# Performance work log

Hardware: AMD Instinct MI355X
Metric: run time of the kernel (lower is better)

The kernel has to match this reference:

```python
import jax, jax.numpy as jnp
import numpy as np

OBS_LEN = 20   # decoder timesteps
NC = 2         # n_coordinates
D = 64         # z_dim + s_dim (LSTM hidden size)
K = 20         # number of latent samples (len(pred_lstm_hidden))
N = 50000      # number of agents
H_MID = 32     # mapping MLP hidden dim


def setup_inputs() -> dict:
    key = jax.random.key(0)
    ks = jax.random.split(key, 8)
    return {
        "obs_traj_rel": jax.random.normal(ks[0], (OBS_LEN, N, NC), jnp.float32),
        "pred_lstm_hidden": jax.random.normal(ks[1], (K, N, D), jnp.float32),
        # mapping MLP: Linear(D->32) + LeakyReLU, Linear(32->D)
        "map_w1": jax.random.normal(ks[2], (H_MID, D), jnp.float32) * 0.1,
        "map_b1": jnp.zeros((H_MID,), jnp.float32),
        "map_w2": jax.random.normal(ks[3], (D, H_MID), jnp.float32) * 0.1,
        "map_b2": jnp.zeros((D,), jnp.float32),
        # LSTMCell params (weights ~ N(0, 0.1), biases zero per _initialize_weights)
        "w_ih": jax.random.normal(ks[4], (4 * D, NC), jnp.float32) * 0.1,
        "w_hh": jax.random.normal(ks[5], (4 * D, D), jnp.float32) * 0.1,
        "b_ih": jnp.zeros((4 * D,), jnp.float32),
        "b_hh": jnp.zeros((4 * D,), jnp.float32),
        # pred_hidden2pos: Linear(D -> NC)
        "pos_w": jax.random.normal(ks[6], (NC, D), jnp.float32) * 0.1,
        "pos_b": jnp.zeros((NC,), jnp.float32),
    }


def _hardsigmoid(x):
    # F.hardsigmoid: relu6(x + 3) / 6
    return jnp.clip(x / 6.0 + 0.5, 0.0, 1.0)


def _hardtanh(x):
    return jnp.clip(x, -1.0, 1.0)


def reference(obs_traj_rel, pred_lstm_hidden, map_w1, map_b1, map_w2, map_b2,
              w_ih, w_hh, b_ih, b_hh, pos_w, pos_b):
    # mapping MLP on initial hidden state: [K, N, D]
    h0 = jax.nn.leaky_relu(pred_lstm_hidden @ map_w1.T + map_b1, negative_slope=0.01)
    h0 = h0 @ map_w2.T + map_b2
    c0 = jnp.zeros_like(h0)

    # input at step i uses obs_traj_rel[max(i-1, 0)]
    idx = jnp.concatenate([jnp.zeros((1,), jnp.int32),
                           jnp.arange(OBS_LEN - 1, dtype=jnp.int32)])
    xs = obs_traj_rel[idx, :, :NC]  # [T, N, NC]

    def step(carry, x_t):
        h, c = carry                                   # [K, N, D]
        xb = jnp.broadcast_to(x_t, (K,) + x_t.shape)   # repeat over samples
        gates = xb @ w_ih.T + b_ih + h @ w_hh.T + b_hh  # [K, N, 4D]
        i_g, f_g, g_g, o_g = jnp.split(gates, 4, axis=-1)
        c_new = _hardsigmoid(f_g) * c + _hardsigmoid(i_g) * _hardtanh(g_g)
        h_new = _hardsigmoid(o_g) * _hardtanh(c_new)
        out = h_new @ pos_w.T + pos_b                  # [K, N, NC]
        return (h_new, c_new), out

    _, outs = jax.lax.scan(step, (h0, c0), xs)
    return outs  # [T, K, N, NC]
```

## Files before the change

kernel.cpp:

```cpp
#include <hip/hip_runtime.h>

#define T_STEPS 20
#define KK      20
#define NW      50000
#define DD      64

typedef __attribute__((ext_vector_type(8))) short bfx8;
typedef __attribute__((ext_vector_type(4))) short sx4;
typedef __attribute__((ext_vector_type(4))) float fx4;
typedef __attribute__((ext_vector_type(2))) float fx2;
typedef __attribute__((ext_vector_type(2))) int   ix2;
typedef __attribute__((ext_vector_type(4))) int   ix4;

__device__ __forceinline__ short f2bf(float f){
  unsigned u = __builtin_bit_cast(unsigned, f);
  return (short)((u + 0x7FFFu + ((u >> 16) & 1u)) >> 16);
}
__device__ __forceinline__ unsigned cvtpk(float lo, float hi){
  unsigned r; asm("v_cvt_pk_bf16_f32 %0, %1, %2" : "=v"(r) : "v"(lo), "v"(hi)); return r;
}
__device__ __forceinline__ float hsig(float x){
  return __builtin_amdgcn_fmed3f(fmaf(x, 0.16666667f, 0.5f), 0.f, 1.f);
}
__device__ __forceinline__ float htanh(float x){
  return __builtin_amdgcn_fmed3f(x, -1.f, 1.f);
}

__device__ __forceinline__ bfx8 frag_f32(const float* p0, const float* p1){
  fx4 lo = *(const fx4*)p0, hi = *(const fx4*)p1;
  bfx8 r;
  r[0]=f2bf(lo[0]); r[1]=f2bf(lo[1]); r[2]=f2bf(lo[2]); r[3]=f2bf(lo[3]);
  r[4]=f2bf(hi[0]); r[5]=f2bf(hi[1]); r[6]=f2bf(hi[2]); r[7]=f2bf(hi[3]);
  return r;
}
__device__ __forceinline__ bfx8 frag_lds(const unsigned short* p0, const unsigned short* p1){
  sx4 lo = *(const sx4*)p0, hi = *(const sx4*)p1;
  bfx8 r;
  r[0]=lo[0]; r[1]=lo[1]; r[2]=lo[2]; r[3]=lo[3];
  r[4]=hi[0]; r[5]=hi[1]; r[6]=hi[2]; r[7]=hi[3];
  return r;
}
__device__ __forceinline__ bfx8 cat(ix2 lo, ix2 hi){
  ix4 t; t[0]=lo[0]; t[1]=lo[1]; t[2]=hi[0]; t[3]=hi[1];
  return __builtin_bit_cast(bfx8, t);
}

#define MFMA(A,B,C) __builtin_amdgcn_mfma_f32_16x16x32_bf16((A),(B),(C),0,0,0)

__global__ __launch_bounds__(256)
void gcrl_fused(const float* __restrict__ obs, const float* __restrict__ pred,
                const float* __restrict__ w1, const float* __restrict__ b1,
                const float* __restrict__ w2, const float* __restrict__ b2,
                const float* __restrict__ wih, const float* __restrict__ whh,
                const float* __restrict__ bih, const float* __restrict__ bhh,
                const float* __restrict__ posw, const float* __restrict__ posb,
                float* __restrict__ out)
{
  __shared__ unsigned short hst[2][2][1152];
  __shared__ unsigned short l1buf[2][16][36];
  __shared__ float xs[19][8][2];

  const int tid = threadIdx.x;
  const int w   = tid >> 6;
  const int l   = tid & 63;
  const int g   = l >> 4;
  const int cc  = l & 15;

  const int bid = blockIdx.x;
  const int k0  = (bid % 5) * 4;
  const int n0  = (bid / 5) * 8;

  for (int i = tid; i < 19 * 16; i += 256){
    int row = i >> 4, rr = i & 15;
    xs[row][rr >> 1][rr & 1] =
      obs[(size_t)row * (NW * 2) + (size_t)(n0 + (rr >> 1)) * 2 + (rr & 1)];
  }

  bfx8 wf[4][2];
  bfx8 a2f[4];
  fx4  bs[4];
  #pragma unroll
  for (int ty = 0; ty < 4; ++ty){
    const int jrow = ty * 64 + w * 16 + cc;
    #pragma unroll
    for (int kt = 0; kt < 2; ++kt)
      wf[ty][kt] = frag_f32(&whh[jrow * DD + kt * 32 + g * 4],
                            &whh[jrow * DD + kt * 32 + 16 + g * 4]);
    unsigned xw = cvtpk(wih[jrow * 2 + 0], wih[jrow * 2 + 1]);
    ix4 t4; t4[0] = (g == 0) ? (int)xw : 0; t4[1] = 0; t4[2] = 0; t4[3] = 0;
    a2f[ty] = __builtin_bit_cast(bfx8, t4);
    const int jreg = ty * 64 + w * 16 + g * 4;
    bs[ty][0] = bih[jreg + 0] + bhh[jreg + 0];
    bs[ty][1] = bih[jreg + 1] + bhh[jreg + 1];
    bs[ty][2] = bih[jreg + 2] + bhh[jreg + 2];
    bs[ty][3] = bih[jreg + 3] + bhh[jreg + 3];
  }
  const int c2 = (cc < 2) ? cc : 0;
  bfx8 pf[2];
  #pragma unroll
  for (int kt = 0; kt < 2; ++kt)
    pf[kt] = frag_f32(&posw[c2 * DD + kt * 32 + g * 4],
                      &posw[c2 * DD + kt * 32 + 16 + g * 4]);
  fx4 pC; pC[0] = posb[0]; pC[1] = posb[1]; pC[2] = 0.f; pC[3] = 0.f;

  float* const outBase =
    out + ((size_t)(k0 + (cc & 3)) * NW + n0 + w * 4 + (cc >> 2)) * 2;

  if (w < 2){
    const int tl = w;
    const int kcell = k0 + (cc & 3);
    const int ncell = n0 + tl * 4 + (cc >> 2);
    const float* Pr = pred + ((size_t)kcell * NW + ncell) * DD;
    bfx8 pa0 = frag_f32(&Pr[g * 4],      &Pr[16 + g * 4]);
    bfx8 pa1 = frag_f32(&Pr[32 + g * 4], &Pr[48 + g * 4]);
    #pragma unroll
    for (int nt = 0; nt < 2; ++nt){
      const int j1 = nt * 16 + cc;
      bfx8 bf0 = frag_f32(&w1[j1 * DD + g * 4],      &w1[j1 * DD + 16 + g * 4]);
      bfx8 bf1 = frag_f32(&w1[j1 * DD + 32 + g * 4], &w1[j1 * DD + 48 + g * 4]);
      const float bb = b1[j1];
      fx4 acc = {bb, bb, bb, bb};
      acc = MFMA(pa0, bf0, acc);
      acc = MFMA(pa1, bf1, acc);
      #pragma unroll
      for (int r = 0; r < 4; ++r){
        float xv = acc[r];
        l1buf[tl][g * 4 + r][nt * 16 + cc] =
          (unsigned short)f2bf(fmaxf(xv, 0.f) + 0.01f * fminf(xv, 0.f));
      }
    }
  }
  __syncthreads();

  #pragma unroll
  for (int tl = 0; tl < 2; ++tl){
    bfx8 bfr = frag_lds(&l1buf[tl][cc][g * 4], &l1buf[tl][cc][16 + g * 4]);
    bfx8 afr = frag_f32(&w2[(w * 16 + cc) * 32 + g * 4],
                        &w2[(w * 16 + cc) * 32 + 16 + g * 4]);
    const int d0 = w * 16 + g * 4;
    fx4 ci; ci[0] = b2[d0]; ci[1] = b2[d0 + 1]; ci[2] = b2[d0 + 2]; ci[3] = b2[d0 + 3];
    fx4 acc = MFMA(afr, bfr, ci);
    ix2 pk;
    pk[0] = (int)cvtpk(acc[0], acc[1]);
    pk[1] = (int)cvtpk(acc[2], acc[3]);
    *(ix2*)&hst[0][tl][cc * 72 + w * 16 + g * 4] = pk;
  }
  float cA0=0.f,cA1=0.f,cA2=0.f,cA3=0.f, cB0=0.f,cB1=0.f,cB2=0.f,cB3=0.f;
  __syncthreads();

  const unsigned short* const rb = &hst[0][0][cc * 72 + g * 4];
  unsigned short*       const wb = &hst[0][0][cc * 72 + w * 16 + g * 4];

#define STEP(XI, TPREV, DOPROJ, RB, WB) do{                                    \
    const int xi_ = (XI);                                                      \
    const fx2 xA = *(const fx2*)&xs[xi_][cc >> 2][0];                          \
    const fx2 xB = *(const fx2*)&xs[xi_][4 + (cc >> 2)][0];                    \
    ix2 lA0 = *(const ix2*)(RB);         ix2 hA0 = *(const ix2*)((RB) + 16);   \
    ix2 lA1 = *(const ix2*)((RB) + 32);  ix2 hA1 = *(const ix2*)((RB) + 48);   \
    ix2 lB0 = *(const ix2*)((RB) + 1152);ix2 hB0 = *(const ix2*)((RB) + 1168); \
    ix2 lB1 = *(const ix2*)((RB) + 1184);ix2 hB1 = *(const ix2*)((RB) + 1200); \
    bfx8 hbA0 = cat(lA0, hA0), hbA1 = cat(lA1, hA1);                           \
    bfx8 hbB0 = cat(lB0, hB0), hbB1 = cat(lB1, hB1);                           \
    unsigned uA = cvtpk(xA[0], xA[1]);                                         \
    unsigned uB = cvtpk(xB[0], xB[1]);                                         \
    ix4 tA4; tA4[0] = (g == 0) ? (int)uA : 0; tA4[1]=0; tA4[2]=0; tA4[3]=0;    \
    ix4 tB4; tB4[0] = (g == 0) ? (int)uB : 0; tB4[1]=0; tB4[2]=0; tB4[3]=0;    \
    bfx8 xbA = __builtin_bit_cast(bfx8, tA4);                                  \
    bfx8 xbB = __builtin_bit_cast(bfx8, tB4);                                  \
    fx4 accA[4], accB[4];                                                      \
    _Pragma("unroll")                                                          \
    for (int ty = 0; ty < 4; ++ty){                                            \
      fx4 aa = MFMA(wf[ty][0], hbA0, bs[ty]);                                  \
      aa = MFMA(wf[ty][1], hbA1, aa);                                          \
      aa = MFMA(a2f[ty], xbA, aa);                                             \
      accA[ty] = aa;                                                           \
      fx4 ab = MFMA(wf[ty][0], hbB0, bs[ty]);                                  \
      ab = MFMA(wf[ty][1], hbB1, ab);                                          \
      ab = MFMA(a2f[ty], xbB, ab);                                             \
      accB[ty] = ab;                                                           \
    }                                                                          \
    if ((DOPROJ) && w < 2){                                                    \
      bfx8 h0 = w ? hbB0 : hbA0;                                               \
      bfx8 h1 = w ? hbB1 : hbA1;                                               \
      fx4 oa = MFMA(pf[0], h0, pC);                                            \
      oa = MFMA(pf[1], h1, oa);                                                \
      if (g == 0){                                                             \
        fx2 ov; ov[0] = oa[0]; ov[1] = oa[1];                                  \
        *(fx2*)(outBase + (size_t)(TPREV) * (KK * NW * 2)) = ov;               \
      }                                                                        \
    }                                                                          \
    {                                                                          \
      float cn0 = fmaf(hsig(accA[1][0]), cA0, hsig(accA[0][0])*htanh(accA[2][0])); \
      float cn1 = fmaf(hsig(accA[1][1]), cA1, hsig(accA[0][1])*htanh(accA[2][1])); \
      float cn2 = fmaf(hsig(accA[1][2]), cA2, hsig(accA[0][2])*htanh(accA[2][2])); \
      float cn3 = fmaf(hsig(accA[1][3]), cA3, hsig(accA[0][3])*htanh(accA[2][3])); \
      cA0=cn0; cA1=cn1; cA2=cn2; cA3=cn3;                                      \
      ix2 pk;                                                                  \
      pk[0] = (int)cvtpk(hsig(accA[3][0])*htanh(cn0), hsig(accA[3][1])*htanh(cn1)); \
      pk[1] = (int)cvtpk(hsig(accA[3][2])*htanh(cn2), hsig(accA[3][3])*htanh(cn3)); \
      *(ix2*)(WB) = pk;                                                        \
    }                                                                          \
    {                                                                          \
      float cn0 = fmaf(hsig(accB[1][0]), cB0, hsig(accB[0][0])*htanh(accB[2][0])); \
      float cn1 = fmaf(hsig(accB[1][1]), cB1, hsig(accB[0][1])*htanh(accB[2][1])); \
      float cn2 = fmaf(hsig(accB[1][2]), cB2, hsig(accB[0][2])*htanh(accB[2][2])); \
      float cn3 = fmaf(hsig(accB[1][3]), cB3, hsig(accB[0][3])*htanh(accB[2][3])); \
      cB0=cn0; cB1=cn1; cB2=cn2; cB3=cn3;                                      \
      ix2 pk;                                                                  \
      pk[0] = (int)cvtpk(hsig(accB[3][0])*htanh(cn0), hsig(accB[3][1])*htanh(cn1)); \
      pk[1] = (int)cvtpk(hsig(accB[3][2])*htanh(cn2), hsig(accB[3][3])*htanh(cn3)); \
      *(ix2*)((WB) + 1152) = pk;                                               \
    }                                                                          \
    __syncthreads();                                                           \
  }while(0)

  for (int t = 0; t < T_STEPS; t += 2){
    STEP((t == 0 ? 0 : t - 1), t - 1, (t > 0), rb,        wb + 2304);
    STEP(t,                    t,     1,       rb + 2304, wb);
  }

  if (w < 2){
    const unsigned short* eb = rb + w * 1152;
    ix2 l0 = *(const ix2*)eb,        h0 = *(const ix2*)(eb + 16);
    ix2 l1 = *(const ix2*)(eb + 32), h1 = *(const ix2*)(eb + 48);
    bfx8 hb0 = cat(l0, h0), hb1 = cat(l1, h1);
    fx4 oa = MFMA(pf[0], hb0, pC);
    oa = MFMA(pf[1], hb1, oa);
    if (g == 0){
      fx2 ov; ov[0] = oa[0]; ov[1] = oa[1];
      *(fx2*)(outBase + (size_t)19 * (KK * NW * 2)) = ov;
    }
  }
#undef STEP
}

extern "C" void kernel_launch(void* const* d_in, const int* in_sizes, int n_in,
                              void* d_out, int out_size, void* d_ws, size_t ws_size,
                              hipStream_t stream){
  const float* obs  = (const float*)d_in[0];
  const float* pred = (const float*)d_in[1];
  const float* w1   = (const float*)d_in[2];
  const float* b1   = (const float*)d_in[3];
  const float* w2   = (const float*)d_in[4];
  const float* b2   = (const float*)d_in[5];
  const float* wih  = (const float*)d_in[6];
  const float* whh  = (const float*)d_in[7];
  const float* bih  = (const float*)d_in[8];
  const float* bhh  = (const float*)d_in[9];
  const float* posw = (const float*)d_in[10];
  const float* posb = (const float*)d_in[11];
  float* o = (float*)d_out;

  dim3 grid(5 * (NW / 8));
  dim3 block(256);
  gcrl_fused<<<grid, block, 0, stream>>>(obs, pred, w1, b1, w2, b2,
                                         wih, whh, bih, bhh, posw, posb, o);
}
```

Before: 1.174 ms.

## Make each wave own a full 16-cell LSTM tile, removing per-step block barriers

Each wave now computes all 256 gate rows for its own 16 (k,n) cells and keeps the full W_hh in registers (32 bf16 fragments). The per-timestep __syncthreads across waves goes away, and the hidden-state exchange becomes wave-private LDS. The bias is folded into the input MFMA through a constant-one column, and each block covers 16 agents, halving the grid. The cost is much higher register pressure: launch_bounds asks for 2 blocks per CU, so spills or lower occupancy are possible, and each wave now issues more MFMAs per step.

```diff
diff --git a/kernel.cpp b/kernel.cpp
--- a/kernel.cpp
+++ b/kernel.cpp
@@ -3,18 +3,17 @@
 #define T_STEPS 20
 #define KK      20
 #define NW      50000
-#define DD      64
 
 typedef __attribute__((ext_vector_type(8))) short bfx8;
 typedef __attribute__((ext_vector_type(4))) short sx4;
 typedef __attribute__((ext_vector_type(4))) float fx4;
 typedef __attribute__((ext_vector_type(2))) float fx2;
+typedef __attribute__((ext_vector_type(4))) int   ix4;
 typedef __attribute__((ext_vector_type(2))) int   ix2;
-typedef __attribute__((ext_vector_type(4))) int   ix4;
-
-__device__ __forceinline__ short f2bf(float f){
+
+__device__ __forceinline__ unsigned f2bfu(float f){
   unsigned u = __builtin_bit_cast(unsigned, f);
-  return (short)((u + 0x7FFFu + ((u >> 16) & 1u)) >> 16);
+  return ((u + 0x7FFFu + ((u >> 16) & 1u)) >> 16);
 }
 __device__ __forceinline__ unsigned cvtpk(float lo, float hi){
   unsigned r; asm("v_cvt_pk_bf16_f32 %0, %1, %2" : "=v"(r) : "v"(lo), "v"(hi)); return r;
@@ -25,12 +24,11 @@
 __device__ __forceinline__ float htanh(float x){
   return __builtin_amdgcn_fmed3f(x, -1.f, 1.f);
 }
-
 __device__ __forceinline__ bfx8 frag_f32(const float* p0, const float* p1){
   fx4 lo = *(const fx4*)p0, hi = *(const fx4*)p1;
   bfx8 r;
-  r[0]=f2bf(lo[0]); r[1]=f2bf(lo[1]); r[2]=f2bf(lo[2]); r[3]=f2bf(lo[3]);
-  r[4]=f2bf(hi[0]); r[5]=f2bf(hi[1]); r[6]=f2bf(hi[2]); r[7]=f2bf(hi[3]);
+  r[0]=(short)f2bfu(lo[0]); r[1]=(short)f2bfu(lo[1]); r[2]=(short)f2bfu(lo[2]); r[3]=(short)f2bfu(lo[3]);
+  r[4]=(short)f2bfu(hi[0]); r[5]=(short)f2bfu(hi[1]); r[6]=(short)f2bfu(hi[2]); r[7]=(short)f2bfu(hi[3]);
   return r;
 }
 __device__ __forceinline__ bfx8 frag_lds(const unsigned short* p0, const unsigned short* p1){
@@ -47,7 +45,7 @@
 
 #define MFMA(A,B,C) __builtin_amdgcn_mfma_f32_16x16x32_bf16((A),(B),(C),0,0,0)
 
-__global__ __launch_bounds__(256)
+__global__ __launch_bounds__(256, 2)
 void gcrl_fused(const float* __restrict__ obs, const float* __restrict__ pred,
                 const float* __restrict__ w1, const float* __restrict__ b1,
                 const float* __restrict__ w2, const float* __restrict__ b2,
@@ -56,9 +54,9 @@
                 const float* __restrict__ posw, const float* __restrict__ posb,
                 float* __restrict__ out)
 {
-  __shared__ unsigned short hst[2][2][1152];
-  __shared__ unsigned short l1buf[2][16][36];
-  __shared__ float xs[19][8][2];
+  __shared__ unsigned short hbuf[4][2][1152];
+  __shared__ unsigned short l1w[4][16][36];
+  __shared__ float xsw[4][19][4][2];
 
   const int tid = threadIdx.x;
   const int w   = tid >> 6;
@@ -68,167 +66,152 @@
 
   const int bid = blockIdx.x;
   const int k0  = (bid % 5) * 4;
-  const int n0  = (bid / 5) * 8;
-
-  for (int i = tid; i < 19 * 16; i += 256){
-    int row = i >> 4, rr = i & 15;
-    xs[row][rr >> 1][rr & 1] =
-      obs[(size_t)row * (NW * 2) + (size_t)(n0 + (rr >> 1)) * 2 + (rr & 1)];
-  }
-
-  bfx8 wf[4][2];
-  bfx8 a2f[4];
-  fx4  bs[4];
+  const int n0b = (bid / 5) * 16;
+
+  const int kc   = k0 + (cc >> 2);
+  const int nc   = n0b + w * 4 + (cc & 3);
+  const int nloc = cc & 3;
+
+  for (int i = l; i < 152; i += 64){
+    const int row = i >> 3, rem = i & 7;
+    xsw[w][row][rem >> 1][rem & 1] =
+      obs[(size_t)row * (NW * 2) + (size_t)(n0b + w * 4 + (rem >> 1)) * 2 + (rem & 1)];
+  }
+
+  bfx8 wf[16][2];
+  bfx8 xa[16];
   #pragma unroll
   for (int ty = 0; ty < 4; ++ty){
-    const int jrow = ty * 64 + w * 16 + cc;
+    #pragma unroll
+    for (int rt = 0; rt < 4; ++rt){
+      const int j = ty * 64 + rt * 16 + cc;
+      #pragma unroll
+      for (int kt = 0; kt < 2; ++kt)
+        wf[ty*4+rt][kt] = frag_f32(&whh[j*64 + kt*32 + 4*g],
+                                   &whh[j*64 + kt*32 + 16 + 4*g]);
+      const unsigned xw = cvtpk(wih[2*j], wih[2*j+1]);
+      const unsigned bw = f2bfu(bih[j] + bhh[j]);
+      ix4 t4;
+      t4[0] = (g == 0) ? (int)xw : 0;
+      t4[1] = (g == 0) ? (int)bw : 0;
+      t4[2] = 0; t4[3] = 0;
+      xa[ty*4+rt] = __builtin_bit_cast(bfx8, t4);
+    }
+  }
+  bfx8 pf[2];
+  {
+    const int c2 = (cc < 2) ? cc : 0;
     #pragma unroll
     for (int kt = 0; kt < 2; ++kt)
-      wf[ty][kt] = frag_f32(&whh[jrow * DD + kt * 32 + g * 4],
-                            &whh[jrow * DD + kt * 32 + 16 + g * 4]);
-    unsigned xw = cvtpk(wih[jrow * 2 + 0], wih[jrow * 2 + 1]);
-    ix4 t4; t4[0] = (g == 0) ? (int)xw : 0; t4[1] = 0; t4[2] = 0; t4[3] = 0;
-    a2f[ty] = __builtin_bit_cast(bfx8, t4);
-    const int jreg = ty * 64 + w * 16 + g * 4;
-    bs[ty][0] = bih[jreg + 0] + bhh[jreg + 0];
-    bs[ty][1] = bih[jreg + 1] + bhh[jreg + 1];
-    bs[ty][2] = bih[jreg + 2] + bhh[jreg + 2];
-    bs[ty][3] = bih[jreg + 3] + bhh[jreg + 3];
-  }
-  const int c2 = (cc < 2) ? cc : 0;
-  bfx8 pf[2];
-  #pragma unroll
-  for (int kt = 0; kt < 2; ++kt)
-    pf[kt] = frag_f32(&posw[c2 * DD + kt * 32 + g * 4],
-                      &posw[c2 * DD + kt * 32 + 16 + g * 4]);
-  fx4 pC; pC[0] = posb[0]; pC[1] = posb[1]; pC[2] = 0.f; pC[3] = 0.f;
-
-  float* const outBase =
-    out + ((size_t)(k0 + (cc & 3)) * NW + n0 + w * 4 + (cc >> 2)) * 2;
-
-  if (w < 2){
-    const int tl = w;
-    const int kcell = k0 + (cc & 3);
-    const int ncell = n0 + tl * 4 + (cc >> 2);
-    const float* Pr = pred + ((size_t)kcell * NW + ncell) * DD;
-    bfx8 pa0 = frag_f32(&Pr[g * 4],      &Pr[16 + g * 4]);
-    bfx8 pa1 = frag_f32(&Pr[32 + g * 4], &Pr[48 + g * 4]);
+      pf[kt] = frag_f32(&posw[c2*64 + kt*32 + 4*g], &posw[c2*64 + kt*32 + 16 + 4*g]);
+  }
+  const fx4 pC = {posb[0], posb[1], 0.f, 0.f};
+
+  {
+    const float* Pr = pred + ((size_t)kc * NW + nc) * 64;
+    bfx8 pa0 = frag_f32(&Pr[4*g],      &Pr[16 + 4*g]);
+    bfx8 pa1 = frag_f32(&Pr[32 + 4*g], &Pr[48 + 4*g]);
     #pragma unroll
     for (int nt = 0; nt < 2; ++nt){
       const int j1 = nt * 16 + cc;
-      bfx8 bf0 = frag_f32(&w1[j1 * DD + g * 4],      &w1[j1 * DD + 16 + g * 4]);
-      bfx8 bf1 = frag_f32(&w1[j1 * DD + 32 + g * 4], &w1[j1 * DD + 48 + g * 4]);
+      bfx8 bf0 = frag_f32(&w1[j1*64 + 4*g],      &w1[j1*64 + 16 + 4*g]);
+      bfx8 bf1 = frag_f32(&w1[j1*64 + 32 + 4*g], &w1[j1*64 + 48 + 4*g]);
       const float bb = b1[j1];
       fx4 acc = {bb, bb, bb, bb};
       acc = MFMA(pa0, bf0, acc);
       acc = MFMA(pa1, bf1, acc);
       #pragma unroll
       for (int r = 0; r < 4; ++r){
-        float xv = acc[r];
-        l1buf[tl][g * 4 + r][nt * 16 + cc] =
-          (unsigned short)f2bf(fmaxf(xv, 0.f) + 0.01f * fminf(xv, 0.f));
+        const float xv = acc[r];
+        l1w[w][g*4 + r][nt*16 + cc] =
+          (unsigned short)f2bfu(fmaxf(xv, 0.f) + 0.01f * fminf(xv, 0.f));
       }
     }
   }
-  __syncthreads();
-
+  {
+    bfx8 bfr = frag_lds(&l1w[w][cc][4*g], &l1w[w][cc][16 + 4*g]);
+    #pragma unroll
+    for (int rt = 0; rt < 4; ++rt){
+      bfx8 afr = frag_f32(&w2[(rt*16 + cc)*32 + 4*g], &w2[(rt*16 + cc)*32 + 16 + 4*g]);
+      fx4 ci = *(const fx4*)&b2[rt*16 + 4*g];
+      fx4 acc = MFMA(afr, bfr, ci);
+      ix2 pk;
+      pk[0] = (int)cvtpk(acc[0], acc[1]);
+      pk[1] = (int)cvtpk(acc[2], acc[3]);
+      *(ix2*)&hbuf[w][0][cc*72 + rt*16 + 4*g] = pk;
+    }
+  }
+
+  float cst[4][4];
   #pragma unroll
-  for (int tl = 0; tl < 2; ++tl){
-    bfx8 bfr = frag_lds(&l1buf[tl][cc][g * 4], &l1buf[tl][cc][16 + g * 4]);
-    bfx8 afr = frag_f32(&w2[(w * 16 + cc) * 32 + g * 4],
-                        &w2[(w * 16 + cc) * 32 + 16 + g * 4]);
-    const int d0 = w * 16 + g * 4;
-    fx4 ci; ci[0] = b2[d0]; ci[1] = b2[d0 + 1]; ci[2] = b2[d0 + 2]; ci[3] = b2[d0 + 3];
-    fx4 acc = MFMA(afr, bfr, ci);
-    ix2 pk;
-    pk[0] = (int)cvtpk(acc[0], acc[1]);
-    pk[1] = (int)cvtpk(acc[2], acc[3]);
-    *(ix2*)&hst[0][tl][cc * 72 + w * 16 + g * 4] = pk;
-  }
-  float cA0=0.f,cA1=0.f,cA2=0.f,cA3=0.f, cB0=0.f,cB1=0.f,cB2=0.f,cB3=0.f;
-  __syncthreads();
-
-  const unsigned short* const rb = &hst[0][0][cc * 72 + g * 4];
-  unsigned short*       const wb = &hst[0][0][cc * 72 + w * 16 + g * 4];
+  for (int a_ = 0; a_ < 4; ++a_)
+    #pragma unroll
+    for (int b_ = 0; b_ < 4; ++b_) cst[a_][b_] = 0.f;
+
+  const unsigned short* const rb0 = &hbuf[w][0][cc*72 + 4*g];
+  const unsigned short* const rb1 = &hbuf[w][1][cc*72 + 4*g];
+  unsigned short* const wb0 = &hbuf[w][0][cc*72 + 4*g];
+  unsigned short* const wb1 = &hbuf[w][1][cc*72 + 4*g];
+
+  float* const outp = out + ((size_t)kc * NW + nc) * 2;
+  const unsigned one_bf = (g == 0) ? 0x00003F80u : 0u;
 
 #define STEP(XI, TPREV, DOPROJ, RB, WB) do{                                    \
-    const int xi_ = (XI);                                                      \
-    const fx2 xA = *(const fx2*)&xs[xi_][cc >> 2][0];                          \
-    const fx2 xB = *(const fx2*)&xs[xi_][4 + (cc >> 2)][0];                    \
-    ix2 lA0 = *(const ix2*)(RB);         ix2 hA0 = *(const ix2*)((RB) + 16);   \
-    ix2 lA1 = *(const ix2*)((RB) + 32);  ix2 hA1 = *(const ix2*)((RB) + 48);   \
-    ix2 lB0 = *(const ix2*)((RB) + 1152);ix2 hB0 = *(const ix2*)((RB) + 1168); \
-    ix2 lB1 = *(const ix2*)((RB) + 1184);ix2 hB1 = *(const ix2*)((RB) + 1200); \
-    bfx8 hbA0 = cat(lA0, hA0), hbA1 = cat(lA1, hA1);                           \
-    bfx8 hbB0 = cat(lB0, hB0), hbB1 = cat(lB1, hB1);                           \
-    unsigned uA = cvtpk(xA[0], xA[1]);                                         \
-    unsigned uB = cvtpk(xB[0], xB[1]);                                         \
-    ix4 tA4; tA4[0] = (g == 0) ? (int)uA : 0; tA4[1]=0; tA4[2]=0; tA4[3]=0;    \
-    ix4 tB4; tB4[0] = (g == 0) ? (int)uB : 0; tB4[1]=0; tB4[2]=0; tB4[3]=0;    \
-    bfx8 xbA = __builtin_bit_cast(bfx8, tA4);                                  \
-    bfx8 xbB = __builtin_bit_cast(bfx8, tB4);                                  \
-    fx4 accA[4], accB[4];                                                      \
-    _Pragma("unroll")                                                          \
-    for (int ty = 0; ty < 4; ++ty){                                            \
-      fx4 aa = MFMA(wf[ty][0], hbA0, bs[ty]);                                  \
-      aa = MFMA(wf[ty][1], hbA1, aa);                                          \
-      aa = MFMA(a2f[ty], xbA, aa);                                             \
-      accA[ty] = aa;                                                           \
-      fx4 ab = MFMA(wf[ty][0], hbB0, bs[ty]);                                  \
-      ab = MFMA(wf[ty][1], hbB1, ab);                                          \
-      ab = MFMA(a2f[ty], xbB, ab);                                             \
-      accB[ty] = ab;                                                           \
-    }                                                                          \
-    if ((DOPROJ) && w < 2){                                                    \
-      bfx8 h0 = w ? hbB0 : hbA0;                                               \
-      bfx8 h1 = w ? hbB1 : hbA1;                                               \
-      fx4 oa = MFMA(pf[0], h0, pC);                                            \
-      oa = MFMA(pf[1], h1, oa);                                                \
+    const fx2 xL = *(const fx2*)&xsw[w][(XI)][nloc][0];                        \
+    const unsigned xw_ = cvtpk(xL[0], xL[1]);                                  \
+    ix4 xb4; xb4[0] = (g==0) ? (int)xw_ : 0; xb4[1] = (int)one_bf;             \
+    xb4[2] = 0; xb4[3] = 0;                                                    \
+    const bfx8 xbf = __builtin_bit_cast(bfx8, xb4);                            \
+    ix2 lA0 = *(const ix2*)(RB);        ix2 hA0 = *(const ix2*)((RB) + 16);    \
+    ix2 lA1 = *(const ix2*)((RB) + 32); ix2 hA1 = *(const ix2*)((RB) + 48);    \
+    bfx8 hb0 = cat(lA0, hA0), hb1 = cat(lA1, hA1);                             \
+    if (DOPROJ){                                                               \
+      fx4 oa = MFMA(pf[0], hb0, pC);                                           \
+      oa = MFMA(pf[1], hb1, oa);                                               \
       if (g == 0){                                                             \
         fx2 ov; ov[0] = oa[0]; ov[1] = oa[1];                                  \
-        *(fx2*)(outBase + (size_t)(TPREV) * (KK * NW * 2)) = ov;               \
+        *(fx2*)(outp + (size_t)(TPREV) * (KK * NW * 2)) = ov;                  \
       }                                                                        \
     }                                                                          \
-    {                                                                          \
-      float cn0 = fmaf(hsig(accA[1][0]), cA0, hsig(accA[0][0])*htanh(accA[2][0])); \
-      float cn1 = fmaf(hsig(accA[1][1]), cA1, hsig(accA[0][1])*htanh(accA[2][1])); \
-      float cn2 = fmaf(hsig(accA[1][2]), cA2, hsig(accA[0][2])*htanh(accA[2][2])); \
-      float cn3 = fmaf(hsig(accA[1][3]), cA3, hsig(accA[0][3])*htanh(accA[2][3])); \
-      cA0=cn0; cA1=cn1; cA2=cn2; cA3=cn3;                                      \
+    _Pragma("unroll")                                                          \
+    for (int rt = 0; rt < 4; ++rt){                                            \
+      const fx4 z = {0.f, 0.f, 0.f, 0.f};                                      \
+      fx4 ai = MFMA(xa[0*4+rt], xbf, z);                                       \
+      ai = MFMA(wf[0*4+rt][0], hb0, ai); ai = MFMA(wf[0*4+rt][1], hb1, ai);    \
+      fx4 af = MFMA(xa[1*4+rt], xbf, z);                                       \
+      af = MFMA(wf[1*4+rt][0], hb0, af); af = MFMA(wf[1*4+rt][1], hb1, af);    \
+      fx4 ag2 = MFMA(xa[2*4+rt], xbf, z);                                      \
+      ag2 = MFMA(wf[2*4+rt][0], hb0, ag2); ag2 = MFMA(wf[2*4+rt][1], hb1, ag2);\
+      fx4 ao = MFMA(xa[3*4+rt], xbf, z);                                       \
+      ao = MFMA(wf[3*4+rt][0], hb0, ao); ao = MFMA(wf[3*4+rt][1], hb1, ao);    \
+      float hq[4];                                                             \
+      _Pragma("unroll")                                                        \
+      for (int r = 0; r < 4; ++r){                                             \
+        const float cn = fmaf(hsig(af[r]), cst[rt][r], hsig(ai[r])*htanh(ag2[r])); \
+        cst[rt][r] = cn;                                                       \
+        hq[r] = hsig(ao[r]) * htanh(cn);                                       \
+      }                                                                        \
       ix2 pk;                                                                  \
-      pk[0] = (int)cvtpk(hsig(accA[3][0])*htanh(cn0), hsig(accA[3][1])*htanh(cn1)); \
-      pk[1] = (int)cvtpk(hsig(accA[3][2])*htanh(cn2), hsig(accA[3][3])*htanh(cn3)); \
-      *(ix2*)(WB) = pk;                                                        \
+      pk[0] = (int)cvtpk(hq[0], hq[1]);                                        \
+      pk[1] = (int)cvtpk(hq[2], hq[3]);                                        \
+      *(ix2*)((WB) + rt*16) = pk;                                              \
     }                                                                          \
-    {                                                                          \
-      float cn0 = fmaf(hsig(accB[1][0]), cB0, hsig(accB[0][0])*htanh(accB[2][0])); \
-      float cn1 = fmaf(hsig(accB[1][1]), cB1, hsig(accB[0][1])*htanh(accB[2][1])); \
-      float cn2 = fmaf(hsig(accB[1][2]), cB2, hsig(accB[0][2])*htanh(accB[2][2])); \
-      float cn3 = fmaf(hsig(accB[1][3]), cB3, hsig(accB[0][3])*htanh(accB[2][3])); \
-      cB0=cn0; cB1=cn1; cB2=cn2; cB3=cn3;                                      \
-      ix2 pk;                                                                  \
-      pk[0] = (int)cvtpk(hsig(accB[3][0])*htanh(cn0), hsig(accB[3][1])*htanh(cn1)); \
-      pk[1] = (int)cvtpk(hsig(accB[3][2])*htanh(cn2), hsig(accB[3][3])*htanh(cn3)); \
-      *(ix2*)((WB) + 1152) = pk;                                               \
-    }                                                                          \
-    __syncthreads();                                                           \
   }while(0)
 
   for (int t = 0; t < T_STEPS; t += 2){
-    STEP((t == 0 ? 0 : t - 1), t - 1, (t > 0), rb,        wb + 2304);
-    STEP(t,                    t,     1,       rb + 2304, wb);
-  }
-
-  if (w < 2){
-    const unsigned short* eb = rb + w * 1152;
-    ix2 l0 = *(const ix2*)eb,        h0 = *(const ix2*)(eb + 16);
-    ix2 l1 = *(const ix2*)(eb + 32), h1 = *(const ix2*)(eb + 48);
+    STEP((t == 0 ? 0 : t - 1), t - 1, (t > 0), rb0, wb1);
+    STEP(t,                    t,     1,       rb1, wb0);
+  }
+
+  {
+    ix2 l0 = *(const ix2*)rb0,        h0 = *(const ix2*)(rb0 + 16);
+    ix2 l1 = *(const ix2*)(rb0 + 32), h1 = *(const ix2*)(rb0 + 48);
     bfx8 hb0 = cat(l0, h0), hb1 = cat(l1, h1);
     fx4 oa = MFMA(pf[0], hb0, pC);
     oa = MFMA(pf[1], hb1, oa);
     if (g == 0){
       fx2 ov; ov[0] = oa[0]; ov[1] = oa[1];
-      *(fx2*)(outBase + (size_t)19 * (KK * NW * 2)) = ov;
+      *(fx2*)(outp + (size_t)19 * (KK * NW * 2)) = ov;
     }
   }
 #undef STEP
@@ -251,7 +234,7 @@
   const float* posb = (const float*)d_in[11];
   float* o = (float*)d_out;
 
-  dim3 grid(5 * (NW / 8));
+  dim3 grid(5 * (NW / 16));
   dim3 block(256);
   gcrl_fused<<<grid, block, 0, stream>>>(obs, pred, w1, b1, w2, b2,
                                          wih, whh, bih, bhh, posw, posb, o);
```

After: 2.129 ms. 81.4% more time.
